# Kernel tuning notes

Hardware: AMD Instinct MI355X
Metric: run time of the kernel (lower is better)

## Reference

```python
import jax, jax.numpy as jnp
import numpy as np

INPUT_SIZE = 500
SENTENCE_SIZE = 128


def setup_inputs() -> dict:
    key = jax.random.key(0)
    ks = jax.random.split(key, 20)
    B, D = 16, 512
    Ho, Hi, Hu = 4, 4, 4
    dh_ori = D // Ho          # 128
    dh = D // (Hi + Hu)       # 64
    s = 0.05
    code = jax.random.normal(ks[0], (B, INPUT_SIZE, D), jnp.float32)
    # binary sentence-membership mask (which code tokens belong to each sentence)
    input_sentence = (jax.random.uniform(ks[1], (B, SENTENCE_SIZE, INPUT_SIZE)) < 0.2).astype(jnp.float32)

    def W(k, h, dout):
        return jax.random.normal(k, (h, D, dout), jnp.float32) * s

    def b(k, h, dout):
        return jax.random.normal(k, (h, dout), jnp.float32) * 0.01

    return dict(
        code=code, input_sentence=input_sentence,
        Wq_ori=W(ks[2], Ho, dh_ori), bq_ori=b(ks[3], Ho, dh_ori),
        Wk_ori=W(ks[4], Ho, dh_ori), bk_ori=b(ks[5], Ho, dh_ori),
        Wq_in=W(ks[6], Hi, dh), bq_in=b(ks[7], Hi, dh),
        Wk_in=W(ks[8], Hi, dh), bk_in=b(ks[9], Hi, dh),
        Wv_in=W(ks[10], Hi, dh), bv_in=b(ks[11], Hi, dh),
        Wq_out=W(ks[12], Hu, dh), bq_out=b(ks[13], Hu, dh),
        Wk_out=W(ks[14], Hu, dh), bk_out=b(ks[15], Hu, dh),
        Wv_out=W(ks[16], Hu, dh), bv_out=b(ks[17], Hu, dh),
    )


def _proj(x, W, b):
    # x: (B, N, D), W: (H, D, F), b: (H, F) -> (B, H, N, F), relu Dense per head
    return jax.nn.relu(jnp.einsum('bnd,hdf->bhnf', x, W) + b[:, None, :])


def reference(code, input_sentence,
              Wq_ori, bq_ori, Wk_ori, bk_ori,
              Wq_in, bq_in, Wk_in, bk_in, Wv_in, bv_in,
              Wq_out, bq_out, Wk_out, bk_out, Wv_out, bv_out):
    B, S = input_sentence.shape[0], input_sentence.shape[1]
    sent = input_sentence

    # ---- original (ori) branch: max over heads of raw QK^T, mask, matmul code ----
    q = _proj(code, Wq_ori, bq_ori)
    k = _proj(code, Wk_ori, bk_ori)
    scores_ori = jnp.einsum('bhnf,bhmf->bhnm', q, k).max(axis=1)      # (B, N, N)
    sA = jnp.einsum('bsn,bnm->bsm', sent, scores_ori)                 # (B, S, N)
    out_ori = jnp.einsum('bsm,bmd->bsd', sent * sA, code)             # (B, S, D)

    # ---- in-mask heads ----
    qi = _proj(code, Wq_in, bq_in)
    ki = _proj(code, Wk_in, bk_in)
    vi = _proj(code, Wv_in, bv_in)
    sc = jnp.einsum('bhnf,bhmf->bhnm', qi, ki)                        # (B, Hi, N, N)
    sAi = jnp.einsum('bsn,bhnm->bhsm', sent, sc)                      # (B, Hi, S, N)
    out_in = jnp.einsum('bhsm,bhmf->bhsf', sent[:, None] * sAi, vi)   # (B, Hi, S, F)

    # ---- out-mask heads ----
    qo = _proj(code, Wq_out, bq_out)
    ko = _proj(code, Wk_out, bk_out)
    vo = _proj(code, Wv_out, bv_out)
    sco = jnp.einsum('bhnf,bhmf->bhnm', qo, ko)
    sAo = jnp.einsum('bsn,bhnm->bhsm', sent, sco)
    masked = (sent - 1.0)[:, None] * sAo                              # (B, Hu, S, N)
    include = sent.sum(axis=2)[:, None, :, None]                      # (B, 1, S, 1)
    masked = masked / (INPUT_SIZE - include) * include
    out_out = jnp.einsum('bhsm,bhmf->bhsf', masked, vo)               # (B, Hu, S, F)

    # original returns a list [ori, in_0..in_Hi-1, out_0..out_Hu-1]; concat along features
    in_flat = jnp.transpose(out_in, (0, 2, 1, 3)).reshape(B, S, -1)
    out_flat = jnp.transpose(out_out, (0, 2, 1, 3)).reshape(B, S, -1)
    return jnp.concatenate([out_ori, in_flat, out_flat], axis=-1)
```

## Files before the change

kernel.cpp:

```cpp
#include <hip/hip_runtime.h>
#include <cfloat>

#define B_  16
#define N_  500
#define NP  512
#define S_  128
#define D_  512
#define FO  128
#define FI  64

typedef unsigned short u16;
typedef __attribute__((ext_vector_type(8))) short bf8;
typedef __attribute__((ext_vector_type(4))) float f4;

#define MFMA(a,b,c) __builtin_amdgcn_mfma_f32_16x16x32_bf16((a),(b),(c),0,0,0)

__device__ __forceinline__ u16 f2b(float x){
    union{float f;unsigned u;} v; v.f=x;
    unsigned r = v.u + 0x7fffu + ((v.u>>16)&1u);
    return (u16)(r>>16);
}
__device__ __forceinline__ float b2f(u16 x){
    union{unsigned u;float f;} v; v.u=((unsigned)x)<<16; return v.f;
}
__device__ __forceinline__ bf8 ldb8(const u16* p){ return *(const bf8*)p; }

__global__ __launch_bounds__(256) void prep_code(const float* __restrict__ code,
                                                 u16* __restrict__ codeB,
                                                 u16* __restrict__ codeT)
{
    __shared__ float T[64][65];
    const int b = blockIdx.x, m0 = blockIdx.y*64, d0 = blockIdx.z*64;
    const int t = threadIdx.x;
    #pragma unroll
    for (int i=0;i<16;++i){
        int idx = t + i*256; int rr = idx>>6, cc = idx&63;
        int m = m0+rr;
        T[rr][cc] = (m < N_) ? code[((size_t)b*N_+m)*D_ + d0+cc] : 0.f;
    }
    __syncthreads();
    #pragma unroll
    for (int i=0;i<16;++i){
        int idx=t+i*256; int rr=idx>>6, cc=idx&63; int m=m0+rr;
        if (m<N_) codeB[((size_t)b*N_+m)*D_ + d0+cc] = f2b(T[rr][cc]);
    }
    #pragma unroll
    for (int i=0;i<16;++i){
        int idx=t+i*256; int dd=idx>>6, mm=idx&63;
        codeT[((size_t)b*D_ + d0+dd)*NP + m0+mm] = f2b(T[mm][dd]);
    }
}

__global__ __launch_bounds__(128) void prep_sent(const float* __restrict__ sent,
                                                 u16* __restrict__ sentB,
                                                 float* __restrict__ inc)
{
    const int b=blockIdx.x, s=blockIdx.y, t=threadIdx.x;
    const float* row = sent + ((size_t)b*S_+s)*N_;
    float4 v = make_float4(0.f,0.f,0.f,0.f);
    const int n = t*4;
    if (n < N_) v = *(const float4*)(row+n);
    float sum = v.x+v.y+v.z+v.w;
    ushort4 o; o.x=f2b(v.x); o.y=f2b(v.y); o.z=f2b(v.z); o.w=f2b(v.w);
    *(ushort4*)&sentB[((size_t)b*S_+s)*NP + n] = o;
    #pragma unroll
    for (int off=32; off; off>>=1) sum += __shfl_down(sum, off);
    __shared__ float ls[2];
    if ((t&63)==0) ls[t>>6]=sum;
    __syncthreads();
    if (t==0) inc[b*S_+s] = ls[0]+ls[1];
}

struct PWAll { const float* W[8]; u16* WT[8]; };
__global__ __launch_bounds__(256) void prep_w_all(PWAll a)
{
    const int slot = blockIdx.y;
    const int widx = slot<4 ? (slot>>1) : slot-2;
    const int ftile= slot<4 ? (slot&1)  : 0;
    const int F    = slot<4 ? 128 : 64;
    const float* W = a.W[widx];
    u16* WT        = a.WT[widx];
    __shared__ float T[64][65];
    const int h=blockIdx.x, f0=ftile*64, d0=blockIdx.z*64, t=threadIdx.x;
    #pragma unroll
    for (int i=0;i<16;++i){
        int idx=t+i*256; int rr=idx>>6, cc=idx&63;
        T[rr][cc] = W[((size_t)h*D_ + d0+rr)*F + f0+cc];
    }
    __syncthreads();
    #pragma unroll
    for (int i=0;i<16;++i){
        int idx=t+i*256; int ff=idx>>6, dd=idx&63;
        WT[((size_t)h*F + f0+ff)*D_ + d0+dd] = f2b(T[dd][ff]);
    }
}

__global__ __launch_bounds__(256) void zero_pad4(u16* a0, u16* a1, u16* a2, u16* a3)
{
    u16* arr4[4] = {a0,a1,a2,a3};
    u16* base = arr4[blockIdx.y] + (size_t)blockIdx.x*FI*NP;
    for (int idx=threadIdx.x; idx<FI*12; idx+=256){
        int f = idx/12, n = N_ + idx%12;
        base[(size_t)f*NP + n] = 0;
    }
}

struct GemmOut { const float* bias[8]; u16* dst[8]; };
__global__ __launch_bounds__(256) void proj_gemm(const u16* __restrict__ codeB,
                                                 const u16* __restrict__ WallT,
                                                 GemmOut go, int ctile0)
{
    __shared__ alignas(16) u16 As[2][128*32];
    __shared__ alignas(16) u16 Bs[2][128*32];
    const int t = threadIdx.x;
    const int w = t>>6, l = t&63, lane16 = l&15, lq = l>>4;
    const int r0 = blockIdx.x*128;
    const int c0 = (blockIdx.y + ctile0)*128;
    const int wr = (w>>1)*64, wc = (w&1)*64;
    const int srow = t>>2, skc = (t&3)*8;

    f4 acc[4][4] = {};
    #pragma unroll
    for (int i=0;i<2;++i){
        const int row = srow + i*64;
        *(bf8*)&As[0][row*32 + skc] = ldb8(codeB + (size_t)(r0+row)*D_ + skc);
        *(bf8*)&Bs[0][row*32 + skc] = ldb8(WallT + (size_t)(c0+row)*D_ + skc);
    }
    __syncthreads();
    int buf = 0;
    for (int k0=0; k0<D_; k0+=32){
        const bool more = (k0+32) < D_;
        bf8 pa[2], pb[2];
        if (more){
            #pragma unroll
            for (int i=0;i<2;++i){
                const int row = srow + i*64;
                pa[i] = ldb8(codeB + (size_t)(r0+row)*D_ + k0+32 + skc);
                pb[i] = ldb8(WallT + (size_t)(c0+row)*D_ + k0+32 + skc);
            }
        }
        bf8 af[4], bfr[4];
        #pragma unroll
        for (int i=0;i<4;++i){
            af[i]  = *(const bf8*)&As[buf][(wr + i*16 + lane16)*32 + lq*8];
            bfr[i] = *(const bf8*)&Bs[buf][(wc + i*16 + lane16)*32 + lq*8];
        }
        #pragma unroll
        for (int i=0;i<4;++i)
            #pragma unroll
            for (int j=0;j<4;++j)
                acc[i][j] = MFMA(af[i], bfr[j], acc[i][j]);
        if (more){
            #pragma unroll
            for (int i=0;i<2;++i){
                const int row = srow + i*64;
                *(bf8*)&As[buf^1][row*32+skc] = pa[i];
                *(bf8*)&Bs[buf^1][row*32+skc] = pb[i];
            }
            __syncthreads();
            buf ^= 1;
        }
    }
    #pragma unroll
    for (int j=0;j<4;++j){
        const int c = c0 + wc + j*16 + lane16;
        int ri, hf, F;
        if (c < 1024){ ri = c>>9; hf = c & 511; F = 128; }
        else { const int u = c-1024; ri = 2 + (u>>8); hf = u & 255; F = 64; }
        const float bv = go.bias[ri][hf];
        const int h  = (F==128) ? (hf>>7) : (hf>>6);
        const int f2 = hf & (F-1);
        const bool tr = (ri>=2) && (ri!=3) && (ri!=6);
        #pragma unroll
        for (int i=0;i<4;++i){
            const int rb = r0 + wr + i*16 + lq*4;
            if (rb >= 8000) continue;
            const int b  = rb / 500;
            const int n0 = rb % 500;
            float v[4];
            #pragma unroll
            for (int reg=0;reg<4;++reg){
                float x = acc[i][j][reg] + bv;
                v[reg] = x>0.f ? x : 0.f;
            }
            if (tr){
                ushort4 o4; o4.x=f2b(v[0]); o4.y=f2b(v[1]); o4.z=f2b(v[2]); o4.w=f2b(v[3]);
                *(ushort4*)&go.dst[ri][((size_t)(b*4+h)*FI + f2)*NP + n0] = o4;
            } else {
                u16* o = go.dst[ri] + ((size_t)(b*4+h)*N_ + n0)*F + f2;
                #pragma unroll
                for (int reg=0;reg<4;++reg) o[(size_t)reg*F] = f2b(v[reg]);
            }
        }
    }
}

__global__ __launch_bounds__(256) void ms_mfma(const u16* __restrict__ q,
                                               const u16* __restrict__ k,
                                               u16* __restrict__ maxscT)
{
    __shared__ alignas(16) u16 Qs[64][136];
    __shared__ alignas(16) u16 Ks[128][136];
    const int t=threadIdx.x, w=t>>6, l=t&63, lane16=l&15, lq=l>>4;
    const int b=blockIdx.x, n0=blockIdx.y*64, m0=blockIdx.z*128;
    const int wr=(w>>1)*32, wc=(w&1)*64;

    f4 best[2][4];
    #pragma unroll
    for(int rt=0;rt<2;++rt)
        #pragma unroll
        for(int ct=0;ct<4;++ct)
            #pragma unroll
            for(int i=0;i<4;++i) best[rt][ct][i] = -FLT_MAX;

    for (int h=0;h<4;++h){
        const u16* qh = q + (size_t)(b*4+h)*N_*FO;
        const u16* kh = k + (size_t)(b*4+h)*N_*FO;
        #pragma unroll
        for (int i=0;i<4;++i){
            const int e=t+i*256, row=e>>4, kc=(e&15)*8;
            int n=n0+row; if(n>N_-1)n=N_-1;
            *(bf8*)&Qs[row][kc] = ldb8(qh + (size_t)n*FO + kc);
        }
        #pragma unroll
        for (int i=0;i<8;++i){
            const int e=t+i*256, row=e>>4, kc=(e&15)*8;
            int m=m0+row; if(m>N_-1)m=N_-1;
            *(bf8*)&Ks[row][kc] = ldb8(kh + (size_t)m*FO + kc);
        }
        __syncthreads();
        f4 acc[2][4]={};
        #pragma unroll
        for (int kk=0;kk<FO;kk+=32){
            bf8 a0=*(const bf8*)&Qs[wr+lane16][kk+lq*8];
            bf8 a1=*(const bf8*)&Qs[wr+16+lane16][kk+lq*8];
            #pragma unroll
            for(int ct=0;ct<4;++ct){
                bf8 bb=*(const bf8*)&Ks[wc+ct*16+lane16][kk+lq*8];
                acc[0][ct]=MFMA(a0,bb,acc[0][ct]);
                acc[1][ct]=MFMA(a1,bb,acc[1][ct]);
            }
        }
        #pragma unroll
        for(int rt=0;rt<2;++rt)
            #pragma unroll
            for(int ct=0;ct<4;++ct)
                #pragma unroll
                for(int i=0;i<4;++i) best[rt][ct][i] = fmaxf(best[rt][ct][i], acc[rt][ct][i]);
        __syncthreads();
    }
    #pragma unroll
    for(int rt=0;rt<2;++rt)
        #pragma unroll
        for(int ct=0;ct<4;++ct){
            const int m  = m0+wc+ct*16+lane16;
            const int nb = n0+wr+rt*16+lq*4;
            if (m < N_ && nb < N_){
                ushort4 o; o.x=f2b(best[rt][ct][0]); o.y=f2b(best[rt][ct][1]);
                o.z=f2b(best[rt][ct][2]); o.w=f2b(best[rt][ct][3]);
                *(ushort4*)&maxscT[((size_t)b*NP+m)*NP + nb] = o;
            }
        }
}

__global__ __launch_bounds__(512) void saoo(const u16* __restrict__ sentB,
                                            const u16* __restrict__ maxscT,
                                            const u16* __restrict__ codeT,
                                            float* __restrict__ out)
{
    __shared__ u16 sAmS[16][520];
    const int b=blockIdx.x, s0=blockIdx.y*16;
    const int t=threadIdx.x, w=t>>6, l=t&63, lane16=l&15, lq=l>>4;

    {
        const int m0 = w*64;
        const u16* ap = sentB + ((size_t)b*S_ + s0+lane16)*NP + lq*8;
        const u16* bp[4];
        #pragma unroll
        for(int ct=0;ct<4;++ct) bp[ct] = maxscT + ((size_t)b*NP + m0+ct*16+lane16)*NP + lq*8;
        f4 acc[4] = {};
        for (int k0=0;k0<NP;k0+=32){
            bf8 av=ldb8(ap+k0);
            #pragma unroll
            for(int ct=0;ct<4;++ct) acc[ct]=MFMA(av, ldb8(bp[ct]+k0), acc[ct]);
        }
        #pragma unroll
        for(int ct=0;ct<4;++ct){
            const int m = m0+ct*16+lane16;
            #pragma unroll
            for(int reg=0;reg<4;++reg){
                const int s = s0+lq*4+reg;
                const float sv = b2f(sentB[((size_t)b*S_+s)*NP+m]);
                sAmS[lq*4+reg][m] = f2b(acc[ct][reg]*sv);
            }
        }
    }
    __syncthreads();
    {
        const int d0 = w*64;
        const u16* bp[4];
        #pragma unroll
        for(int ct=0;ct<4;++ct) bp[ct] = codeT + ((size_t)b*D_ + d0+ct*16+lane16)*NP + lq*8;
        f4 acc[4] = {};
        for (int k0=0;k0<NP;k0+=32){
            bf8 av = *(const bf8*)&sAmS[lane16][k0+lq*8];
            #pragma unroll
            for(int ct=0;ct<4;++ct) acc[ct]=MFMA(av, ldb8(bp[ct]+k0), acc[ct]);
        }
        #pragma unroll
        for(int ct=0;ct<4;++ct){
            const int d = d0+ct*16+lane16;
            #pragma unroll
            for(int reg=0;reg<4;++reg){
                const int s = s0+lq*4+reg;
                out[((size_t)b*S_+s)*1024 + d] = acc[ct][reg];
            }
        }
    }
}

struct AttnArgs { const u16* qT[2]; const u16* kp[2]; const u16* vT[2]; };
__global__ __launch_bounds__(256) void attn_fused(AttnArgs a,
                                                  const u16* __restrict__ sentB,
                                                  const float* __restrict__ inc,
                                                  float* __restrict__ out)
{
    __shared__ float red[4][32][68];
    __shared__ u16 qsS[32][72];
    __shared__ u16 Pw[4][32][72];
    const int bh=blockIdx.x, b=bh>>2, h=bh&3, s0=blockIdx.y*32, br=blockIdx.z;
    const u16* qT = a.qT[br];
    const u16* kp = a.kp[br];
    const u16* vT = a.vT[br];
    const int t=threadIdx.x, w=t>>6, l=t&63, lane16=l&15, lq=l>>4;

    {
        const u16 *ap[2], *bp[4];
        #pragma unroll
        for(int rt=0;rt<2;++rt) ap[rt] = sentB + ((size_t)b*S_ + s0+rt*16+lane16)*NP + w*128 + lq*8;
        #pragma unroll
        for(int ct=0;ct<4;++ct) bp[ct] = qT + ((size_t)bh*FI + ct*16+lane16)*NP + w*128 + lq*8;
        f4 acc[2][4] = {};
        #pragma unroll
        for (int k0=0;k0<128;k0+=32){
            bf8 a0=ldb8(ap[0]+k0), a1=ldb8(ap[1]+k0);
            #pragma unroll
            for(int ct=0;ct<4;++ct){
                bf8 bb=ldb8(bp[ct]+k0);
                acc[0][ct]=MFMA(a0,bb,acc[0][ct]);
                acc[1][ct]=MFMA(a1,bb,acc[1][ct]);
            }
        }
        #pragma unroll
        for(int rt=0;rt<2;++rt)
            #pragma unroll
            for(int ct=0;ct<4;++ct)
                #pragma unroll
                for(int reg=0;reg<4;++reg)
                    red[w][rt*16+lq*4+reg][ct*16+lane16] = acc[rt][ct][reg];
    }
    __syncthreads();
    {
        const int s=t>>3, f0=(t&7)*8;
        #pragma unroll
        for (int j=0;j<8;++j){
            float v = red[0][s][f0+j]+red[1][s][f0+j]+red[2][s][f0+j]+red[3][s][f0+j];
            qsS[s][f0+j] = f2b(v);
        }
    }
    __syncthreads();

    f4 accO[2][4] = {};
    #pragma unroll
    for (int c=0;c<2;++c){
        const int m0 = w*64 + c*256;
        f4 p[2][4] = {};
        const u16* bp[4];
        #pragma unroll
        for(int ct=0;ct<4;++ct){
            int m=m0+ct*16+lane16; if(m>N_-1)m=N_-1;
            bp[ct] = kp + ((size_t)bh*N_+m)*FI + lq*8;
        }
        #pragma unroll
        for (int kk=0; kk<FI; kk+=32){
            bf8 a0 = *(const bf8*)&qsS[lane16][kk+lq*8];
            bf8 a1 = *(const bf8*)&qsS[16+lane16][kk+lq*8];
            #pragma unroll
            for(int ct=0;ct<4;++ct){
                bf8 bb=ldb8(bp[ct]+kk);
                p[0][ct]=MFMA(a0,bb,p[0][ct]);
                p[1][ct]=MFMA(a1,bb,p[1][ct]);
            }
        }
        #pragma unroll
        for(int rt=0;rt<2;++rt)
            #pragma unroll
            for(int ct=0;ct<4;++ct){
                const int m = m0+ct*16+lane16;
                #pragma unroll
                for(int reg=0;reg<4;++reg){
                    const int s = s0+rt*16+lq*4+reg;
                    const float sv = b2f(sentB[((size_t)b*S_+s)*NP+m]);
                    const float wgt = br ? ((m<N_)? sv-1.f : 0.f) : sv;
                    Pw[w][rt*16+lq*4+reg][ct*16+lane16] = f2b(p[rt][ct][reg]*wgt);
                }
            }
        #pragma unroll
        for (int kk2=0; kk2<64; kk2+=32){
            bf8 a2[2];
            #pragma unroll
            for(int rt=0;rt<2;++rt) a2[rt] = *(const bf8*)&Pw[w][rt*16+lane16][kk2+lq*8];
            #pragma unroll
            for(int ct=0;ct<4;++ct){
                bf8 vv = ldb8(vT + ((size_t)bh*FI + ct*16+lane16)*NP + m0+kk2+lq*8);
                accO[0][ct]=MFMA(a2[0],vv,accO[0][ct]);
                accO[1][ct]=MFMA(a2[1],vv,accO[1][ct]);
            }
        }
    }
    #pragma unroll
    for(int rt=0;rt<2;++rt)
        #pragma unroll
        for(int ct=0;ct<4;++ct)
            #pragma unroll
            for(int reg=0;reg<4;++reg)
                red[w][rt*16+lq*4+reg][ct*16+lane16] = accO[rt][ct][reg];
    __syncthreads();
    {
        const int s=t>>3, f0=(t&7)*8;
        float fac = 1.f;
        if (br){ const float ic = inc[b*S_+s0+s]; fac = ic/(500.f-ic); }
        const size_t o = ((size_t)b*S_+s0+s)*1024 + (br?768:512) + h*FI + f0;
        #pragma unroll
        for (int j=0;j<8;++j){
            float v = red[0][s][f0+j]+red[1][s][f0+j]+red[2][s][f0+j]+red[3][s][f0+j];
            out[o+j] = v*fac;
        }
    }
}

extern "C" void kernel_launch(void* const* d_in, const int* in_sizes, int n_in,
                              void* d_out, int out_size, void* d_ws, size_t ws_size,
                              hipStream_t stream)
{
    const float* code   = (const float*)d_in[0];
    const float* sent   = (const float*)d_in[1];
    const float* Wq_ori = (const float*)d_in[2];
    const float* bq_ori = (const float*)d_in[3];
    const float* Wk_ori = (const float*)d_in[4];
    const float* bk_ori = (const float*)d_in[5];
    const float* Wq_in  = (const float*)d_in[6];
    const float* bq_in  = (const float*)d_in[7];
    const float* Wk_in  = (const float*)d_in[8];
    const float* bk_in  = (const float*)d_in[9];
    const float* Wv_in  = (const float*)d_in[10];
    const float* bv_in  = (const float*)d_in[11];
    const float* Wq_out = (const float*)d_in[12];
    const float* bq_out = (const float*)d_in[13];
    const float* Wk_out = (const float*)d_in[14];
    const float* bk_out = (const float*)d_in[15];
    const float* Wv_out = (const float*)d_in[16];
    const float* bv_out = (const float*)d_in[17];
    float* out = (float*)d_out;

    char* w = (char*)d_ws;
    u16*   codeB  = (u16*)(w);
    u16*   WallT  = (u16*)(w + 8257536);
    u16*   WTqo   = WallT;
    u16*   WTko   = WallT +  262144;
    u16*   WTqi   = WallT +  524288;
    u16*   WTki   = WallT +  655360;
    u16*   WTvi   = WallT +  786432;
    u16*   WTqu   = WallT +  917504;
    u16*   WTku   = WallT + 1048576;
    u16*   WTvu   = WallT + 1179648;
    u16*   sentB  = (u16*)(w + 10878976);
    float* incp   = (float*)(w + 12976128);
    char*  S      = w + 12984320;
    u16* q_ori  = (u16*)(S);
    u16* k_ori  = (u16*)(S + 8192000);
    u16* maxscT = (u16*)(S + 16384000);
    u16* codeT  = (u16*)(S + 24772608);
    u16* k_in   = (u16*)(S);
    u16* k_out  = (u16*)(S + 4096000);
    u16* qT_in  = (u16*)(S + 8192000);
    u16* qT_out = (u16*)(S + 12386304);
    u16* vT_in  = (u16*)(S + 16580608);
    u16* vT_out = (u16*)(S + 20774912);

    prep_code<<<dim3(16,8,8), 256, 0, stream>>>(code, codeB, codeT);
    prep_sent<<<dim3(16,128), 128, 0, stream>>>(sent, sentB, incp);
    PWAll pw;
    pw.W[0]=Wq_ori; pw.W[1]=Wk_ori; pw.W[2]=Wq_in; pw.W[3]=Wk_in;
    pw.W[4]=Wv_in;  pw.W[5]=Wq_out; pw.W[6]=Wk_out; pw.W[7]=Wv_out;
    pw.WT[0]=WTqo; pw.WT[1]=WTko; pw.WT[2]=WTqi; pw.WT[3]=WTki;
    pw.WT[4]=WTvi; pw.WT[5]=WTqu; pw.WT[6]=WTku; pw.WT[7]=WTvu;
    prep_w_all<<<dim3(4,10,8), 256, 0, stream>>>(pw);

    GemmOut go;
    go.bias[0]=bq_ori; go.bias[1]=bk_ori; go.bias[2]=bq_in; go.bias[3]=bk_in;
    go.bias[4]=bv_in;  go.bias[5]=bq_out; go.bias[6]=bk_out; go.bias[7]=bv_out;
    go.dst[0]=q_ori; go.dst[1]=k_ori; go.dst[2]=qT_in; go.dst[3]=k_in;
    go.dst[4]=vT_in; go.dst[5]=qT_out; go.dst[6]=k_out; go.dst[7]=vT_out;

    proj_gemm<<<dim3(63,8), 256, 0, stream>>>(codeB, WallT, go, 0);
    ms_mfma<<<dim3(16,8,4), 256, 0, stream>>>(q_ori, k_ori, maxscT);
    saoo<<<dim3(16,8), 512, 0, stream>>>(sentB, maxscT, codeT, out);

    zero_pad4<<<dim3(64,4), 256, 0, stream>>>(qT_in, qT_out, vT_in, vT_out);
    proj_gemm<<<dim3(63,12), 256, 0, stream>>>(codeB, WallT, go, 8);

    AttnArgs aa;
    aa.qT[0]=qT_in;  aa.qT[1]=qT_out;
    aa.kp[0]=k_in;   aa.kp[1]=k_out;
    aa.vT[0]=vT_in;  aa.vT[1]=vT_out;
    attn_fused<<<dim3(64,4,2), 256, 0, stream>>>(aa, sentB, incp, out);
}
```

Measured before the change: 136.4 us.

## Merge projection GEMMs into one launch and stage tiles via direct global-to-LDS loads

```diff
diff --git a/kernel.cpp b/kernel.cpp
--- a/kernel.cpp
+++ b/kernel.cpp
@@ -24,6 +24,12 @@
     union{unsigned u;float f;} v; v.u=((unsigned)x)<<16; return v.f;
 }
 __device__ __forceinline__ bf8 ldb8(const u16* p){ return *(const bf8*)p; }
+
+__device__ __forceinline__ void gl2lds16(const u16* g, u16* lds){
+    __builtin_amdgcn_global_load_lds(
+        (const __attribute__((address_space(1))) unsigned int*)g,
+        (__attribute__((address_space(3))) unsigned int*)lds, 16, 0, 0);
+}
 
 __global__ __launch_bounds__(256) void prep_code(const float* __restrict__ code,
                                                  u16* __restrict__ codeB,
@@ -108,37 +114,34 @@
 struct GemmOut { const float* bias[8]; u16* dst[8]; };
 __global__ __launch_bounds__(256) void proj_gemm(const u16* __restrict__ codeB,
                                                  const u16* __restrict__ WallT,
-                                                 GemmOut go, int ctile0)
+                                                 GemmOut go)
 {
     __shared__ alignas(16) u16 As[2][128*32];
     __shared__ alignas(16) u16 Bs[2][128*32];
     const int t = threadIdx.x;
     const int w = t>>6, l = t&63, lane16 = l&15, lq = l>>4;
     const int r0 = blockIdx.x*128;
-    const int c0 = (blockIdx.y + ctile0)*128;
+    const int c0 = blockIdx.y*128;
     const int wr = (w>>1)*64, wc = (w&1)*64;
-    const int srow = t>>2, skc = (t&3)*8;
+    const int srow = l>>2;
+    const int scol = (l&3)*8;
 
     f4 acc[4][4] = {};
-    #pragma unroll
-    for (int i=0;i<2;++i){
-        const int row = srow + i*64;
-        *(bf8*)&As[0][row*32 + skc] = ldb8(codeB + (size_t)(r0+row)*D_ + skc);
-        *(bf8*)&Bs[0][row*32 + skc] = ldb8(WallT + (size_t)(c0+row)*D_ + skc);
-    }
-    __syncthreads();
+
+    auto STAGE = [&](int buf, int k0){
+        #pragma unroll
+        for (int iss=0; iss<2; ++iss){
+            const int rbase = w*32 + iss*16;
+            gl2lds16(codeB + (size_t)(r0+rbase+srow)*D_ + k0 + scol, &As[buf][rbase*32]);
+            gl2lds16(WallT + (size_t)(c0+rbase+srow)*D_ + k0 + scol, &Bs[buf][rbase*32]);
+        }
+    };
+
+    STAGE(0, 0);
     int buf = 0;
     for (int k0=0; k0<D_; k0+=32){
-        const bool more = (k0+32) < D_;
-        bf8 pa[2], pb[2];
-        if (more){
-            #pragma unroll
-            for (int i=0;i<2;++i){
-                const int row = srow + i*64;
-                pa[i] = ldb8(codeB + (size_t)(r0+row)*D_ + k0+32 + skc);
-                pb[i] = ldb8(WallT + (size_t)(c0+row)*D_ + k0+32 + skc);
-            }
-        }
+        __syncthreads();
+        if (k0+32 < D_) STAGE(buf^1, k0+32);
         bf8 af[4], bfr[4];
         #pragma unroll
         for (int i=0;i<4;++i){
@@ -150,16 +153,7 @@
             #pragma unroll
             for (int j=0;j<4;++j)
                 acc[i][j] = MFMA(af[i], bfr[j], acc[i][j]);
-        if (more){
-            #pragma unroll
-            for (int i=0;i<2;++i){
-                const int row = srow + i*64;
-                *(bf8*)&As[buf^1][row*32+skc] = pa[i];
-                *(bf8*)&Bs[buf^1][row*32+skc] = pb[i];
-            }
-            __syncthreads();
-            buf ^= 1;
-        }
+        buf ^= 1;
     }
     #pragma unroll
     for (int j=0;j<4;++j){
@@ -476,17 +470,16 @@
     u16*   WTvu   = WallT + 1179648;
     u16*   sentB  = (u16*)(w + 10878976);
     float* incp   = (float*)(w + 12976128);
-    char*  S      = w + 12984320;
-    u16* q_ori  = (u16*)(S);
-    u16* k_ori  = (u16*)(S + 8192000);
-    u16* maxscT = (u16*)(S + 16384000);
-    u16* codeT  = (u16*)(S + 24772608);
-    u16* k_in   = (u16*)(S);
-    u16* k_out  = (u16*)(S + 4096000);
-    u16* qT_in  = (u16*)(S + 8192000);
-    u16* qT_out = (u16*)(S + 12386304);
-    u16* vT_in  = (u16*)(S + 16580608);
-    u16* vT_out = (u16*)(S + 20774912);
+    u16* q_ori  = (u16*)(w + 12984320);
+    u16* k_ori  = (u16*)(w + 21176320);
+    u16* maxscT = (u16*)(w + 29368320);
+    u16* codeT  = (u16*)(w + 37756928);
+    u16* k_in   = (u16*)(w + 46145536);
+    u16* k_out  = (u16*)(w + 50241536);
+    u16* qT_in  = (u16*)(w + 54337536);
+    u16* qT_out = (u16*)(w + 58531840);
+    u16* vT_in  = (u16*)(w + 62726144);
+    u16* vT_out = (u16*)(w + 66920448);
 
     prep_code<<<dim3(16,8,8), 256, 0, stream>>>(code, codeB, codeT);
     prep_sent<<<dim3(16,128), 128, 0, stream>>>(sent, sentB, incp);
@@ -496,19 +489,17 @@
     pw.WT[0]=WTqo; pw.WT[1]=WTko; pw.WT[2]=WTqi; pw.WT[3]=WTki;
     pw.WT[4]=WTvi; pw.WT[5]=WTqu; pw.WT[6]=WTku; pw.WT[7]=WTvu;
     prep_w_all<<<dim3(4,10,8), 256, 0, stream>>>(pw);
+    zero_pad4<<<dim3(64,4), 256, 0, stream>>>(qT_in, qT_out, vT_in, vT_out);
 
     GemmOut go;
     go.bias[0]=bq_ori; go.bias[1]=bk_ori; go.bias[2]=bq_in; go.bias[3]=bk_in;
     go.bias[4]=bv_in;  go.bias[5]=bq_out; go.bias[6]=bk_out; go.bias[7]=bv_out;
     go.dst[0]=q_ori; go.dst[1]=k_ori; go.dst[2]=qT_in; go.dst[3]=k_in;
     go.dst[4]=vT_in; go.dst[5]=qT_out; go.dst[6]=k_out; go.dst[7]=vT_out;
-
-    proj_gemm<<<dim3(63,8), 256, 0, stream>>>(codeB, WallT, go, 0);
+    proj_gemm<<<dim3(63,20), 256, 0, stream>>>(codeB, WallT, go);
+
     ms_mfma<<<dim3(16,8,4), 256, 0, stream>>>(q_ori, k_ori, maxscT);
     saoo<<<dim3(16,8), 512, 0, stream>>>(sentB, maxscT, codeT, out);
-
-    zero_pad4<<<dim3(64,4), 256, 0, stream>>>(qT_in, qT_out, vT_in, vT_out);
-    proj_gemm<<<dim3(63,12), 256, 0, stream>>>(codeB, WallT, go, 8);
 
     AttnArgs aa;
     aa.qT[0]=qT_in;  aa.qT[1]=qT_out;
```

Measured after the change: 136.9 us. Within noise of the previous version (+0.4%).
